# Optimization experiments

Measured on AMD Instinct MI355X. Metric: run time of the kernel, lower is better.

## Reference

```python
import jax, jax.numpy as jnp
import numpy as np
import math

NUM_HEADS = 32
NUM_KV = 8
D = 128          # num_hidden == per-head dim in this module
S = 2048
B = 1
DK = 128
ROPE_BASE = 10000.0


def rope(x):
    # x: [B, H, S, D]; standard Llama-style RoPE (split-halves rotation) over positions.
    d = x.shape[-1]
    half = d // 2
    pos = jnp.arange(x.shape[2], dtype=jnp.float32)                       # [S]
    inv_freq = 1.0 / (ROPE_BASE ** (jnp.arange(half, dtype=jnp.float32) / half))
    ang = pos[:, None] * inv_freq[None, :]                                # [S, half]
    cos = jnp.cos(ang)
    sin = jnp.sin(ang)
    x1 = x[..., :half]
    x2 = x[..., half:]
    return jnp.concatenate([x1 * cos - x2 * sin, x1 * sin + x2 * cos], axis=-1)


def setup_inputs() -> dict:
    key = jax.random.key(0)
    ks = jax.random.split(key, 8)
    query = jax.random.normal(ks[0], (B, S, D), dtype=jnp.float32)
    k_in = jax.random.normal(ks[1], (B, S, D), dtype=jnp.float32)
    v_in = jax.random.normal(ks[2], (B, S, D), dtype=jnp.float32)
    # causal mask: 1 where attention allowed (lower triangle incl diagonal)
    mask = jnp.tril(jnp.ones((S, S), dtype=jnp.int32))[None, None]        # [1,1,S,S]
    sc = 0.02
    Wq = jax.random.normal(ks[3], (NUM_HEADS * D, D), dtype=jnp.float32) * sc
    bq = jnp.zeros((NUM_HEADS * D,), dtype=jnp.float32)
    Wk = jax.random.normal(ks[4], (NUM_KV * D, D), dtype=jnp.float32) * sc
    bk = jnp.zeros((NUM_KV * D,), dtype=jnp.float32)
    Wv = jax.random.normal(ks[5], (NUM_KV * D, D), dtype=jnp.float32) * sc
    bv = jnp.zeros((NUM_KV * D,), dtype=jnp.float32)
    Wo = jax.random.normal(ks[6], (D, NUM_HEADS * D), dtype=jnp.float32) * sc
    bo = jnp.zeros((D,), dtype=jnp.float32)
    return {"query": query, "key": k_in, "values": v_in, "mask": mask,
            "Wq": Wq, "bq": bq, "Wk": Wk, "bk": bk, "Wv": Wv, "bv": bv,
            "Wo": Wo, "bo": bo}


def reference(query, key, values, mask, Wq, bq, Wk, bk, Wv, bv, Wo, bo):
    Bq, Sq, Dh = query.shape
    # projections; torch Linear: x @ W.T + b. Note: view (reshape), not transpose,
    # exactly as in the original module.
    q = (query @ Wq.T + bq).reshape(Bq, NUM_HEADS, Sq, Dh)   # [B,H,S,D]
    k = (key @ Wk.T + bk).reshape(Bq, NUM_KV, Sq, Dh)        # [B,Hkv,S,D]
    v = (values @ Wv.T + bv).reshape(Bq, NUM_KV, Sq, Dh)
    rk = rope(k)
    rv = rope(v)  # module applies RoPE to values too (faithful)
    rep = NUM_HEADS // NUM_KV
    # torch .repeat((1, rep, 1, 1)) tiles whole head blocks -> jnp.tile
    rk = jnp.tile(rk, (1, rep, 1, 1))                        # [B,H,S,D]
    rv = jnp.tile(rv, (1, rep, 1, 1))
    scores = jnp.einsum('bhqd,bhkd->bhqk', q, rk) / math.sqrt(DK)
    scores = jnp.where(mask == 0, -jnp.inf, scores)
    attn = jax.nn.softmax(scores, axis=-1)
    out = jnp.einsum('bhqk,bhkd->bhqd', attn, rv)            # [B,H,S,D]
    out = out.transpose(0, 2, 1, 3).reshape(Bq, Sq, NUM_HEADS * Dh)
    return out @ Wo.T + bo
```

## Files before the change

### kernel.cpp

```cpp
#include <hip/hip_runtime.h>

typedef unsigned short u16;
typedef unsigned int u32;
typedef short frag_t __attribute__((ext_vector_type(8)));
typedef float f32x4 __attribute__((ext_vector_type(4)));

#define S_LEN 2048

__device__ __forceinline__ float bf2f(u32 u) {
  union { u32 i; float f; } v; v.i = u << 16; return v.f;
}
__device__ __forceinline__ u16 f2bf(float f) {
  u32 x = __float_as_uint(f);
  u32 r = (x + 0x7fffu + ((x >> 16) & 1u)) >> 16;
  return (u16)r;
}
__device__ __forceinline__ void unpack8(uint4 r, float* o) {
  o[0] = bf2f(r.x & 0xffffu); o[1] = bf2f(r.x >> 16);
  o[2] = bf2f(r.y & 0xffffu); o[3] = bf2f(r.y >> 16);
  o[4] = bf2f(r.z & 0xffffu); o[5] = bf2f(r.z >> 16);
  o[6] = bf2f(r.w & 0xffffu); o[7] = bf2f(r.w >> 16);
}
__device__ __forceinline__ u16 ld_in(const void* p, size_t idx, bool fp32) {
  if (fp32) return f2bf(((const float*)p)[idx]);
  return ((const u16*)p)[idx];
}
__device__ __forceinline__ uint4 ld8(const void* p, size_t eidx, bool fp32) {
  if (!fp32) return *(const uint4*)((const u16*)p + eidx);
  const float4* f = (const float4*)((const float*)p + eidx);
  float4 x = f[0], y = f[1];
  uint4 r;
  r.x = (u32)f2bf(x.x) | ((u32)f2bf(x.y) << 16);
  r.y = (u32)f2bf(x.z) | ((u32)f2bf(x.w) << 16);
  r.z = (u32)f2bf(y.x) | ((u32)f2bf(y.y) << 16);
  r.w = (u32)f2bf(y.z) | ((u32)f2bf(y.w) << 16);
  return r;
}

__global__ __launch_bounds__(256) void proj_all(
    const void* __restrict__ query, const void* __restrict__ key,
    const void* __restrict__ values,
    const void* __restrict__ Wq, const void* __restrict__ bq,
    const void* __restrict__ Wk, const void* __restrict__ bk,
    const void* __restrict__ Wv, const void* __restrict__ bv,
    u16* __restrict__ Qb, u16* __restrict__ Kb, u16* __restrict__ Vtmp,
    u32* __restrict__ flag_out) {
  __shared__ u16 As[128][136];
  __shared__ u16 Ws[128][136];
  __shared__ u32 flagS;
  u16 (*Cs)[136] = As;
  const int t = threadIdx.x;
  if (t < 64) {
    u32 e = ((u32)((const u16*)query)[2 * t] >> 7) & 0xFFu;
    bool ok = (e >= 110u && e <= 140u);
    unsigned long long b = __ballot(ok);
    if (t == 0) flagS = (__popcll(b) < 32) ? 1u : 0u;
  }
  __syncthreads();
  const bool fp32 = (flagS != 0u);
  if (t == 0 && blockIdx.x == 0 && blockIdx.y == 0) *flag_out = flagS;
  const int x = blockIdx.x;
  const void *A, *W, *bias;
  u16* C; int N, n0;
  if (x < 32)      { A = query;  W = Wq; bias = bq; C = Qb;   N = 4096; n0 = x << 7; }
  else if (x < 40) { A = key;    W = Wk; bias = bk; C = Kb;   N = 1024; n0 = (x - 32) << 7; }
  else             { A = values; W = Wv; bias = bv; C = Vtmp; N = 1024; n0 = (x - 40) << 7; }
  const float osc = (x < 32) ? 0.12751743f : 1.0f;
  const int m0 = blockIdx.y << 7;
#pragma unroll
  for (int i = 0; i < 8; ++i) {
    int task = t + (i << 8);
    int row = task >> 4, ch = (task & 15) << 3;
    *(uint4*)&As[row][ch] = ld8(A, (size_t)(m0 + row) * 128 + ch, fp32);
    *(uint4*)&Ws[row][ch] = ld8(W, (size_t)(n0 + row) * 128 + ch, fp32);
  }
  __syncthreads();
  const int lane = t & 63, w = t >> 6, quad = lane >> 4, l15 = lane & 15;
  const int rm = (w & 1) << 6, rn = (w >> 1) << 6;
  f32x4 acc[4][4];
#pragma unroll
  for (int mt = 0; mt < 4; ++mt)
#pragma unroll
    for (int nt = 0; nt < 4; ++nt) acc[mt][nt] = 0.f;
#pragma unroll
  for (int mtp = 0; mtp < 2; ++mtp) {
    frag_t a0[4], a1[4];
#pragma unroll
    for (int kc = 0; kc < 4; ++kc) {
      a0[kc] = *(const frag_t*)&As[rm + mtp * 32 + l15][kc * 32 + quad * 8];
      a1[kc] = *(const frag_t*)&As[rm + mtp * 32 + 16 + l15][kc * 32 + quad * 8];
    }
#pragma unroll
    for (int nt = 0; nt < 4; ++nt)
#pragma unroll
      for (int kc = 0; kc < 4; ++kc) {
        frag_t b = *(const frag_t*)&Ws[rn + nt * 16 + l15][kc * 32 + quad * 8];
        acc[mtp * 2][nt] = __builtin_amdgcn_mfma_f32_16x16x32_bf16(a0[kc], b, acc[mtp * 2][nt], 0, 0, 0);
        acc[mtp * 2 + 1][nt] = __builtin_amdgcn_mfma_f32_16x16x32_bf16(a1[kc], b, acc[mtp * 2 + 1][nt], 0, 0, 0);
      }
  }
  __syncthreads();
#pragma unroll
  for (int nt = 0; nt < 4; ++nt) {
    float bb = bf2f((u32)ld_in(bias, n0 + rn + nt * 16 + l15, fp32));
#pragma unroll
    for (int mt = 0; mt < 4; ++mt) {
      int row = rm + ((mt >> 1) * 32) + ((mt & 1) * 16) + quad * 4;
#pragma unroll
      for (int r = 0; r < 4; ++r)
        Cs[row + r][rn + nt * 16 + l15] = f2bf((acc[mt][nt][r] + bb) * osc);
    }
  }
  __syncthreads();
#pragma unroll
  for (int i = 0; i < 8; ++i) {
    int task = t + (i << 8);
    int row = task >> 4, ch = (task & 15) << 3;
    *(uint4*)&C[(size_t)(m0 + row) * N + n0 + ch] = *(const uint4*)&Cs[row][ch];
  }
}

__global__ __launch_bounds__(256) void rope_kv_tr(u16* __restrict__ Kb,
                                                  const u16* __restrict__ Vb,
                                                  u16* __restrict__ VbT) {
  __shared__ u16 Lt[128][72];
  const int t = threadIdx.x;
  const int s0 = blockIdx.x << 6;
  const int g = blockIdx.y;
  for (int i = t; i < 4096; i += 256) {
    int s = s0 + (i >> 6), ii = i & 63;
    float invf = __expf(-(float)ii * 0.14391156831212787f);
    float ang = (float)s * invf;
    float sn, cs;
    sincosf(ang, &sn, &cs);
    size_t base = ((size_t)(g << 11) + s) * 128 + ii;
    float k1 = bf2f((u32)Kb[base]), k2 = bf2f((u32)Kb[base + 64]);
    Kb[base] = f2bf(k1 * cs - k2 * sn);
    Kb[base + 64] = f2bf(k1 * sn + k2 * cs);
  }
  const u16* src = Vb + (size_t)g * S_LEN * 128;
  for (int i = t; i < 512; i += 256) {
    int r = i >> 3, d8 = (i & 7) << 3;
    float lo[8], hi[8];
    unpack8(*(const uint4*)&src[(size_t)(s0 + r) * 128 + d8], lo);
    unpack8(*(const uint4*)&src[(size_t)(s0 + r) * 128 + d8 + 64], hi);
#pragma unroll
    for (int j = 0; j < 8; ++j) {
      float invf = __expf(-(float)(d8 + j) * 0.14391156831212787f);
      float ang = (float)(s0 + r) * invf;
      float sn, cs;
      sincosf(ang, &sn, &cs);
      Lt[d8 + j][r] = f2bf(lo[j] * cs - hi[j] * sn);
      Lt[d8 + 64 + j][r] = f2bf(lo[j] * sn + hi[j] * cs);
    }
  }
  __syncthreads();
  u16* dst = VbT + (size_t)g * 128 * S_LEN + s0;
  for (int i = t; i < 2048; i += 256) {
    int d = i >> 4, s4 = (i & 15) << 2;
    uint2 pk;
    pk.x = (u32)Lt[d][s4] | ((u32)Lt[d][s4 + 1] << 16);
    pk.y = (u32)Lt[d][s4 + 2] | ((u32)Lt[d][s4 + 3] << 16);
    *(uint2*)&dst[(size_t)d * S_LEN + s4] = pk;
  }
}

__global__ __launch_bounds__(256) void attn_mfma(
    const u16* __restrict__ Qb, const u16* __restrict__ Kb,
    const u16* __restrict__ VbT, u16* __restrict__ OpA, u16* __restrict__ OpB,
    float2* __restrict__ Ml, int nkh) {
  __shared__ union SmemU {
    struct { u16 Kt[32][136]; u16 Vt[128][40]; u16 St[128][40]; } m;
    struct { u16 Og[128][136]; } e;
  } su;
  const int t = threadIdx.x;
  const int lane = t & 63, w = t >> 6, quad = lane >> 4, l15 = lane & 15;
  const int g = (int)blockIdx.x & 7;
  const int kh = (int)blockIdx.x >> 3;
  const int h = g + (w << 3);
  const u16* Kg = Kb + (size_t)g * S_LEN * 128;
  const u16* Vg = VbT + (size_t)g * 128 * S_LEN;
  const int kR = t >> 4, kC = (t & 15) << 3;
  const int vR = t >> 2, vC = (t & 3) << 3;
  u16* dst = kh ? OpB : OpA;

  const int qt = 63 - (int)blockIdx.y;
  const int q0 = qt << 5;
  const int niter = qt + 1;
  frag_t aq[2][4];
#pragma unroll
  for (int qp = 0; qp < 2; ++qp)
#pragma unroll
    for (int kc = 0; kc < 4; ++kc)
      aq[qp][kc] = *(const frag_t*)&Qb[((size_t)h * S_LEN + q0 + qp * 16 + l15) * 128 +
                                       kc * 32 + quad * 8];
  float m_r[2] = {-1e30f, -1e30f}, l_r[2] = {0.f, 0.f};
  f32x4 oacc[2][8];
#pragma unroll
  for (int qp = 0; qp < 2; ++qp)
#pragma unroll
    for (int nt = 0; nt < 8; ++nt) oacc[qp][nt] = 0.f;

  uint4 kpf[2], vpf[2];
  if (kh < niter) {
    const int k0 = kh << 5;
    kpf[0] = *(const uint4*)&Kg[(size_t)(k0 + kR) * 128 + kC];
    kpf[1] = *(const uint4*)&Kg[(size_t)(k0 + kR + 16) * 128 + kC];
    vpf[0] = *(const uint4*)&Vg[(size_t)vR * S_LEN + k0 + vC];
    vpf[1] = *(const uint4*)&Vg[(size_t)(vR + 64) * S_LEN + k0 + vC];
  }
  for (int sj = kh; sj < niter; sj += nkh) {
    const int k0 = sj << 5;
    __syncthreads();
    *(uint4*)&su.m.Kt[kR][kC] = kpf[0];
    *(uint4*)&su.m.Kt[kR + 16][kC] = kpf[1];
    *(uint4*)&su.m.Vt[vR][vC] = vpf[0];
    *(uint4*)&su.m.Vt[vR + 64][vC] = vpf[1];
    __syncthreads();
    if (sj + nkh < niter) {
      const int kn = (sj + nkh) << 5;
      kpf[0] = *(const uint4*)&Kg[(size_t)(kn + kR) * 128 + kC];
      kpf[1] = *(const uint4*)&Kg[(size_t)(kn + kR + 16) * 128 + kC];
      vpf[0] = *(const uint4*)&Vg[(size_t)vR * S_LEN + kn + vC];
      vpf[1] = *(const uint4*)&Vg[(size_t)(vR + 64) * S_LEN + kn + vC];
    }
    f32x4 s4[2][2];
#pragma unroll
    for (int kk = 0; kk < 2; ++kk) { s4[kk][0] = 0.f; s4[kk][1] = 0.f; }
#pragma unroll
    for (int kc = 0; kc < 4; ++kc)
#pragma unroll
      for (int kk = 0; kk < 2; ++kk) {
        frag_t a = *(const frag_t*)&su.m.Kt[kk * 16 + l15][kc * 32 + quad * 8];
        s4[kk][0] = __builtin_amdgcn_mfma_f32_16x16x32_bf16(a, aq[0][kc], s4[kk][0], 0, 0, 0);
        s4[kk][1] = __builtin_amdgcn_mfma_f32_16x16x32_bf16(a, aq[1][kc], s4[kk][1], 0, 0, 0);
      }
    const bool lastm = (sj == niter - 1);
    float alpha[2];
#pragma unroll
    for (int qp = 0; qp < 2; ++qp) {
      const int qg = q0 + qp * 16 + l15;
      float mx = -1e30f;
#pragma unroll
      for (int kk = 0; kk < 2; ++kk)
#pragma unroll
        for (int r = 0; r < 4; ++r) {
          float sv = s4[kk][qp][r];
          if (lastm && (k0 + kk * 16 + quad * 4 + r) > qg) sv = -1e30f;
          s4[kk][qp][r] = sv;
          mx = fmaxf(mx, sv);
        }
      mx = fmaxf(mx, __shfl_xor(mx, 16));
      mx = fmaxf(mx, __shfl_xor(mx, 32));
      float mn = fmaxf(m_r[qp], mx);
      alpha[qp] = __builtin_amdgcn_exp2f(m_r[qp] - mn);
      m_r[qp] = mn;
      float sum = 0.f;
      const int strow = w * 32 + qp * 16 + l15;
#pragma unroll
      for (int kk = 0; kk < 2; ++kk) {
        float p0 = __builtin_amdgcn_exp2f(s4[kk][qp][0] - mn);
        float p1 = __builtin_amdgcn_exp2f(s4[kk][qp][1] - mn);
        float p2 = __builtin_amdgcn_exp2f(s4[kk][qp][2] - mn);
        float p3 = __builtin_amdgcn_exp2f(s4[kk][qp][3] - mn);
        sum += (p0 + p1) + (p2 + p3);
        uint2 pk;
        pk.x = (u32)f2bf(p0) | ((u32)f2bf(p1) << 16);
        pk.y = (u32)f2bf(p2) | ((u32)f2bf(p3) << 16);
        *(uint2*)&su.m.St[strow][kk * 16 + quad * 4] = pk;
      }
      sum += __shfl_xor(sum, 16);
      sum += __shfl_xor(sum, 32);
      l_r[qp] = l_r[qp] * alpha[qp] + sum;
    }
    if (__any(alpha[0] < 1.0f || alpha[1] < 1.0f)) {
#pragma unroll
      for (int qp = 0; qp < 2; ++qp)
#pragma unroll
        for (int r = 0; r < 4; ++r) {
          float al = __shfl(alpha[qp], quad * 4 + r);
#pragma unroll
          for (int nt = 0; nt < 8; ++nt) oacc[qp][nt][r] *= al;
        }
    }
    frag_t pa0 = *(const frag_t*)&su.m.St[w * 32 + l15][quad * 8];
    frag_t pa1 = *(const frag_t*)&su.m.St[w * 32 + 16 + l15][quad * 8];
#pragma unroll
    for (int nt = 0; nt < 8; ++nt) {
      frag_t v = *(const frag_t*)&su.m.Vt[nt * 16 + l15][quad * 8];
      oacc[0][nt] = __builtin_amdgcn_mfma_f32_16x16x32_bf16(pa0, v, oacc[0][nt], 0, 0, 0);
      oacc[1][nt] = __builtin_amdgcn_mfma_f32_16x16x32_bf16(pa1, v, oacc[1][nt], 0, 0, 0);
    }
  }
  __syncthreads();
#pragma unroll
  for (int qp = 0; qp < 2; ++qp)
#pragma unroll
    for (int r = 0; r < 4; ++r) {
      float fac = 1.0f;
      if (nkh == 1) fac = 1.0f / __shfl(l_r[qp], quad * 4 + r);
      int row = w * 32 + qp * 16 + quad * 4 + r;
#pragma unroll
      for (int nt = 0; nt < 8; ++nt)
        su.e.Og[row][nt * 16 + l15] = f2bf(oacc[qp][nt][r] * fac);
    }
  __syncthreads();
#pragma unroll
  for (int jj = 0; jj < 8; ++jj) {
    int c = t + (jj << 8);
    int row = c >> 4, ch = (c & 15) << 3;
    int hh = row >> 5, qr = row & 31;
    *(uint4*)&dst[(size_t)(q0 + qr) * 4096 + (g + hh * 8) * 128 + ch] =
        *(const uint4*)&su.e.Og[row][ch];
  }
  if (nkh == 2 && quad == 0) {
#pragma unroll
    for (int qp = 0; qp < 2; ++qp)
      Ml[((size_t)kh * 32 + h) * S_LEN + q0 + qp * 16 + l15] =
          make_float2(m_r[qp], l_r[qp]);
  }
}

__global__ __launch_bounds__(256) void out_part(
    const u16* __restrict__ OpA, const u16* __restrict__ OpB,
    const float2* __restrict__ Ml, const void* __restrict__ Wo,
    float* __restrict__ Pout, const u32* __restrict__ flagp, int nkh) {
  __shared__ u16 As[128][136];
  __shared__ u16 Ws[128][136];
  const bool fp32 = (*flagp != 0u);
  const int t = threadIdx.x;
  const int lane = t & 63, w = t >> 6, quad = lane >> 4, l15 = lane & 15;
  const int rm = (w & 1) << 6, rn = (w >> 1) << 6;
  const int m0 = (int)blockIdx.x << 7;
  const int z = (int)blockIdx.y;
  f32x4 acc[4][4];
#pragma unroll
  for (int mt = 0; mt < 4; ++mt)
#pragma unroll
    for (int nt = 0; nt < 4; ++nt) acc[mt][nt] = 0.f;
  for (int kc2 = 0; kc2 < 2; ++kc2) {
    if (kc2) __syncthreads();
    const int kc0 = (z << 8) + (kc2 << 7);
    const int hh = kc0 >> 7;
#pragma unroll
    for (int i = 0; i < 8; ++i) {
      int task = t + (i << 8);
      int row = task >> 4, ch = (task & 15) << 3;
      size_t idx = (size_t)(m0 + row) * 4096 + kc0 + ch;
      if (nkh == 2) {
        int s = m0 + row;
        float2 p1 = Ml[(size_t)hh * S_LEN + s];
        float2 p2 = Ml[(size_t)(32 + hh) * S_LEN + s];
        float mn = fmaxf(p1.x, p2.x);
        float a1 = __builtin_amdgcn_exp2f(p1.x - mn);
        float a2 = __builtin_amdgcn_exp2f(p2.x - mn);
        float linv = 1.0f / (a1 * p1.y + a2 * p2.y);
        float w1 = a1 * linv, w2 = a2 * linv;
        float o1[8], o2[8];
        unpack8(*(const uint4*)&OpA[idx], o1);
        unpack8(*(const uint4*)&OpB[idx], o2);
        uint4 r;
        r.x = (u32)f2bf(o1[0] * w1 + o2[0] * w2) | ((u32)f2bf(o1[1] * w1 + o2[1] * w2) << 16);
        r.y = (u32)f2bf(o1[2] * w1 + o2[2] * w2) | ((u32)f2bf(o1[3] * w1 + o2[3] * w2) << 16);
        r.z = (u32)f2bf(o1[4] * w1 + o2[4] * w2) | ((u32)f2bf(o1[5] * w1 + o2[5] * w2) << 16);
        r.w = (u32)f2bf(o1[6] * w1 + o2[6] * w2) | ((u32)f2bf(o1[7] * w1 + o2[7] * w2) << 16);
        *(uint4*)&As[row][ch] = r;
      } else {
        *(uint4*)&As[row][ch] = *(const uint4*)&OpA[idx];
      }
      *(uint4*)&Ws[row][ch] = ld8(Wo, (size_t)row * 4096 + kc0 + ch, fp32);
    }
    __syncthreads();
#pragma unroll
    for (int mtp = 0; mtp < 2; ++mtp) {
      frag_t a0[4], a1[4];
#pragma unroll
      for (int kc = 0; kc < 4; ++kc) {
        a0[kc] = *(const frag_t*)&As[rm + mtp * 32 + l15][kc * 32 + quad * 8];
        a1[kc] = *(const frag_t*)&As[rm + mtp * 32 + 16 + l15][kc * 32 + quad * 8];
      }
#pragma unroll
      for (int nt = 0; nt < 4; ++nt)
#pragma unroll
        for (int kc = 0; kc < 4; ++kc) {
          frag_t b = *(const frag_t*)&Ws[rn + nt * 16 + l15][kc * 32 + quad * 8];
          acc[mtp * 2][nt] = __builtin_amdgcn_mfma_f32_16x16x32_bf16(a0[kc], b, acc[mtp * 2][nt], 0, 0, 0);
          acc[mtp * 2 + 1][nt] = __builtin_amdgcn_mfma_f32_16x16x32_bf16(a1[kc], b, acc[mtp * 2 + 1][nt], 0, 0, 0);
        }
    }
  }
#pragma unroll
  for (int mt = 0; mt < 4; ++mt) {
    int mrow = m0 + rm + ((mt >> 1) * 32) + ((mt & 1) * 16) + quad * 4;
#pragma unroll
    for (int nt = 0; nt < 4; ++nt) {
      int n = rn + nt * 16 + l15;
#pragma unroll
      for (int r = 0; r < 4; ++r)
        Pout[((size_t)z * 2048 + mrow + r) * 128 + n] = acc[mt][nt][r];
    }
  }
}

__global__ __launch_bounds__(256) void out_red(
    const float* __restrict__ Pout, const void* __restrict__ bo,
    void* __restrict__ out, const u32* __restrict__ flagp) {
  const bool fp32 = (*flagp != 0u);
  int e4 = blockIdx.x * 256 + threadIdx.x;
  const float4* P = (const float4*)Pout;
  float4 s = P[e4];
#pragma unroll
  for (int z = 1; z < 16; ++z) {
    float4 p = P[(size_t)z * 65536 + e4];
    s.x += p.x; s.y += p.y; s.z += p.z; s.w += p.w;
  }
  int n = (e4 << 2) & 127;
  s.x += bf2f((u32)ld_in(bo, n + 0, fp32));
  s.y += bf2f((u32)ld_in(bo, n + 1, fp32));
  s.z += bf2f((u32)ld_in(bo, n + 2, fp32));
  s.w += bf2f((u32)ld_in(bo, n + 3, fp32));
  if (fp32) {
    ((float4*)out)[e4] = s;
  } else {
    uint2 pk;
    pk.x = (u32)f2bf(s.x) | ((u32)f2bf(s.y) << 16);
    pk.y = (u32)f2bf(s.z) | ((u32)f2bf(s.w) << 16);
    *(uint2*)((u16*)out + (e4 << 2)) = pk;
  }
}

extern "C" void kernel_launch(void* const* d_in, const int* in_sizes, int n_in,
                              void* d_out, int out_size, void* d_ws, size_t ws_size,
                              hipStream_t stream) {
  (void)in_sizes; (void)n_in; (void)out_size;
  const void* query  = d_in[0];
  const void* key    = d_in[1];
  const void* values = d_in[2];
  const void* Wq = d_in[4];
  const void* bq = d_in[5];
  const void* Wk = d_in[6];
  const void* bk = d_in[7];
  const void* Wv = d_in[8];
  const void* bv = d_in[9];
  const void* Wo = d_in[10];
  const void* bo = d_in[11];

  char* ws = (char*)d_ws;
  u32* flag   = (u32*)ws;
  u16* Qb     = (u16*)(ws + 64);
  u16* Kb     = (u16*)(ws + 64 + (16ull << 20));
  u16* VbT    = (u16*)(ws + 64 + (20ull << 20));
  u16* Vtmp   = (u16*)(ws + 64 + (24ull << 20));
  u16* Ob     = (u16*)(ws + 64 + (24ull << 20));
  u16* OpB    = (u16*)(ws + 64 + (40ull << 20));
  float2* Mlb = (float2*)(ws + 64 + (56ull << 20));
  float* Pout = (float*)Qb;

  const bool split = (ws_size >= (58ull << 20));
  const int nkh = split ? 2 : 1;

  proj_all<<<dim3(48, 16), 256, 0, stream>>>(query, key, values, Wq, bq, Wk, bk,
                                             Wv, bv, Qb, Kb, Vtmp, flag);
  rope_kv_tr<<<dim3(32, 8), 256, 0, stream>>>(Kb, Vtmp, VbT);
  attn_mfma<<<dim3(8 * nkh, 64), 256, 0, stream>>>(Qb, Kb, VbT, Ob, OpB, Mlb, nkh);
  out_part<<<dim3(16, 16), 256, 0, stream>>>(Ob, OpB, Mlb, Wo, Pout, flag, nkh);
  out_red<<<256, 256, 0, stream>>>(Pout, bo, d_out, flag);
}
```

Before: 248.3 us.

## Pair causal query tiles per attention block, halve out_part tile, use packed bf16 convert

Each attention block now processes two query tiles (qt and 63-qt) in sequence so every block does a balanced amount of causal work, and the grid is halved. Launch bounds request two blocks per SM. The output projection kernel uses 64-row M tiles with twice as many blocks to improve occupancy. Software bf16 rounding is replaced with the hardware v_cvt_pk_bf16_f32 packed conversion. The trade-off is fewer attention blocks, which lowers parallelism and adds a serial second pass inside each block.

```diff
diff --git a/kernel.cpp b/kernel.cpp
--- a/kernel.cpp
+++ b/kernel.cpp
@@ -14,6 +14,11 @@
   u32 x = __float_as_uint(f);
   u32 r = (x + 0x7fffu + ((x >> 16) & 1u)) >> 16;
   return (u16)r;
+}
+__device__ __forceinline__ u32 pkbf(float lo, float hi) {
+  u32 r;
+  asm("v_cvt_pk_bf16_f32 %0, %1, %2" : "=v"(r) : "v"(lo), "v"(hi));
+  return r;
 }
 __device__ __forceinline__ void unpack8(uint4 r, float* o) {
   o[0] = bf2f(r.x & 0xffffu); o[1] = bf2f(r.x >> 16);
@@ -30,10 +35,10 @@
   const float4* f = (const float4*)((const float*)p + eidx);
   float4 x = f[0], y = f[1];
   uint4 r;
-  r.x = (u32)f2bf(x.x) | ((u32)f2bf(x.y) << 16);
-  r.y = (u32)f2bf(x.z) | ((u32)f2bf(x.w) << 16);
-  r.z = (u32)f2bf(y.x) | ((u32)f2bf(y.y) << 16);
-  r.w = (u32)f2bf(y.z) | ((u32)f2bf(y.w) << 16);
+  r.x = pkbf(x.x, x.y);
+  r.y = pkbf(x.z, x.w);
+  r.z = pkbf(y.x, y.y);
+  r.w = pkbf(y.z, y.w);
   return r;
 }
 
@@ -165,7 +170,7 @@
   }
 }
 
-__global__ __launch_bounds__(256) void attn_mfma(
+__global__ __launch_bounds__(256, 2) void attn_mfma(
     const u16* __restrict__ Qb, const u16* __restrict__ Kb,
     const u16* __restrict__ VbT, u16* __restrict__ OpA, u16* __restrict__ OpB,
     float2* __restrict__ Ml, int nkh) {
@@ -177,6 +182,7 @@
   const int lane = t & 63, w = t >> 6, quad = lane >> 4, l15 = lane & 15;
   const int g = (int)blockIdx.x & 7;
   const int kh = (int)blockIdx.x >> 3;
+  const int pi = (int)blockIdx.y;
   const int h = g + (w << 3);
   const u16* Kg = Kb + (size_t)g * S_LEN * 128;
   const u16* Vg = VbT + (size_t)g * 128 * S_LEN;
@@ -184,140 +190,142 @@
   const int vR = t >> 2, vC = (t & 3) << 3;
   u16* dst = kh ? OpB : OpA;
 
-  const int qt = 63 - (int)blockIdx.y;
-  const int q0 = qt << 5;
-  const int niter = qt + 1;
-  frag_t aq[2][4];
-#pragma unroll
-  for (int qp = 0; qp < 2; ++qp)
-#pragma unroll
-    for (int kc = 0; kc < 4; ++kc)
-      aq[qp][kc] = *(const frag_t*)&Qb[((size_t)h * S_LEN + q0 + qp * 16 + l15) * 128 +
-                                       kc * 32 + quad * 8];
-  float m_r[2] = {-1e30f, -1e30f}, l_r[2] = {0.f, 0.f};
-  f32x4 oacc[2][8];
-#pragma unroll
-  for (int qp = 0; qp < 2; ++qp)
-#pragma unroll
-    for (int nt = 0; nt < 8; ++nt) oacc[qp][nt] = 0.f;
-
-  uint4 kpf[2], vpf[2];
-  if (kh < niter) {
-    const int k0 = kh << 5;
-    kpf[0] = *(const uint4*)&Kg[(size_t)(k0 + kR) * 128 + kC];
-    kpf[1] = *(const uint4*)&Kg[(size_t)(k0 + kR + 16) * 128 + kC];
-    vpf[0] = *(const uint4*)&Vg[(size_t)vR * S_LEN + k0 + vC];
-    vpf[1] = *(const uint4*)&Vg[(size_t)(vR + 64) * S_LEN + k0 + vC];
-  }
-  for (int sj = kh; sj < niter; sj += nkh) {
-    const int k0 = sj << 5;
+  for (int tp = 0; tp < 2; ++tp) {
+    const int qt = tp ? pi : 63 - pi;
+    const int q0 = qt << 5;
+    const int niter = qt + 1;
+    frag_t aq[2][4];
+#pragma unroll
+    for (int qp = 0; qp < 2; ++qp)
+#pragma unroll
+      for (int kc = 0; kc < 4; ++kc)
+        aq[qp][kc] = *(const frag_t*)&Qb[((size_t)h * S_LEN + q0 + qp * 16 + l15) * 128 +
+                                         kc * 32 + quad * 8];
+    float m_r[2] = {-1e30f, -1e30f}, l_r[2] = {0.f, 0.f};
+    f32x4 oacc[2][8];
+#pragma unroll
+    for (int qp = 0; qp < 2; ++qp)
+#pragma unroll
+      for (int nt = 0; nt < 8; ++nt) oacc[qp][nt] = 0.f;
+
+    uint4 kpf[2], vpf[2];
+    if (kh < niter) {
+      const int k0 = kh << 5;
+      kpf[0] = *(const uint4*)&Kg[(size_t)(k0 + kR) * 128 + kC];
+      kpf[1] = *(const uint4*)&Kg[(size_t)(k0 + kR + 16) * 128 + kC];
+      vpf[0] = *(const uint4*)&Vg[(size_t)vR * S_LEN + k0 + vC];
+      vpf[1] = *(const uint4*)&Vg[(size_t)(vR + 64) * S_LEN + k0 + vC];
+    }
+    for (int sj = kh; sj < niter; sj += nkh) {
+      const int k0 = sj << 5;
+      __syncthreads();
+      *(uint4*)&su.m.Kt[kR][kC] = kpf[0];
+      *(uint4*)&su.m.Kt[kR + 16][kC] = kpf[1];
+      *(uint4*)&su.m.Vt[vR][vC] = vpf[0];
+      *(uint4*)&su.m.Vt[vR + 64][vC] = vpf[1];
+      __syncthreads();
+      if (sj + nkh < niter) {
+        const int kn = (sj + nkh) << 5;
+        kpf[0] = *(const uint4*)&Kg[(size_t)(kn + kR) * 128 + kC];
+        kpf[1] = *(const uint4*)&Kg[(size_t)(kn + kR + 16) * 128 + kC];
+        vpf[0] = *(const uint4*)&Vg[(size_t)vR * S_LEN + kn + vC];
+        vpf[1] = *(const uint4*)&Vg[(size_t)(vR + 64) * S_LEN + kn + vC];
+      }
+      f32x4 s4[2][2];
+#pragma unroll
+      for (int kk = 0; kk < 2; ++kk) { s4[kk][0] = 0.f; s4[kk][1] = 0.f; }
+#pragma unroll
+      for (int kc = 0; kc < 4; ++kc)
+#pragma unroll
+        for (int kk = 0; kk < 2; ++kk) {
+          frag_t a = *(const frag_t*)&su.m.Kt[kk * 16 + l15][kc * 32 + quad * 8];
+          s4[kk][0] = __builtin_amdgcn_mfma_f32_16x16x32_bf16(a, aq[0][kc], s4[kk][0], 0, 0, 0);
+          s4[kk][1] = __builtin_amdgcn_mfma_f32_16x16x32_bf16(a, aq[1][kc], s4[kk][1], 0, 0, 0);
+        }
+      const bool lastm = (sj == niter - 1);
+      float alpha[2];
+#pragma unroll
+      for (int qp = 0; qp < 2; ++qp) {
+        const int qg = q0 + qp * 16 + l15;
+        float mx = -1e30f;
+#pragma unroll
+        for (int kk = 0; kk < 2; ++kk)
+#pragma unroll
+          for (int r = 0; r < 4; ++r) {
+            float sv = s4[kk][qp][r];
+            if (lastm && (k0 + kk * 16 + quad * 4 + r) > qg) sv = -1e30f;
+            s4[kk][qp][r] = sv;
+            mx = fmaxf(mx, sv);
+          }
+        mx = fmaxf(mx, __shfl_xor(mx, 16));
+        mx = fmaxf(mx, __shfl_xor(mx, 32));
+        float mn = fmaxf(m_r[qp], mx);
+        alpha[qp] = __builtin_amdgcn_exp2f(m_r[qp] - mn);
+        m_r[qp] = mn;
+        float sum = 0.f;
+        const int strow = w * 32 + qp * 16 + l15;
+#pragma unroll
+        for (int kk = 0; kk < 2; ++kk) {
+          float p0 = __builtin_amdgcn_exp2f(s4[kk][qp][0] - mn);
+          float p1 = __builtin_amdgcn_exp2f(s4[kk][qp][1] - mn);
+          float p2 = __builtin_amdgcn_exp2f(s4[kk][qp][2] - mn);
+          float p3 = __builtin_amdgcn_exp2f(s4[kk][qp][3] - mn);
+          sum += (p0 + p1) + (p2 + p3);
+          uint2 pk;
+          pk.x = pkbf(p0, p1);
+          pk.y = pkbf(p2, p3);
+          *(uint2*)&su.m.St[strow][kk * 16 + quad * 4] = pk;
+        }
+        sum += __shfl_xor(sum, 16);
+        sum += __shfl_xor(sum, 32);
+        l_r[qp] = l_r[qp] * alpha[qp] + sum;
+      }
+      if (__any(alpha[0] < 1.0f || alpha[1] < 1.0f)) {
+#pragma unroll
+        for (int qp = 0; qp < 2; ++qp)
+#pragma unroll
+          for (int r = 0; r < 4; ++r) {
+            float al = __shfl(alpha[qp], quad * 4 + r);
+#pragma unroll
+            for (int nt = 0; nt < 8; ++nt) oacc[qp][nt][r] *= al;
+          }
+      }
+      frag_t pa0 = *(const frag_t*)&su.m.St[w * 32 + l15][quad * 8];
+      frag_t pa1 = *(const frag_t*)&su.m.St[w * 32 + 16 + l15][quad * 8];
+#pragma unroll
+      for (int nt = 0; nt < 8; ++nt) {
+        frag_t v = *(const frag_t*)&su.m.Vt[nt * 16 + l15][quad * 8];
+        oacc[0][nt] = __builtin_amdgcn_mfma_f32_16x16x32_bf16(pa0, v, oacc[0][nt], 0, 0, 0);
+        oacc[1][nt] = __builtin_amdgcn_mfma_f32_16x16x32_bf16(pa1, v, oacc[1][nt], 0, 0, 0);
+      }
+    }
     __syncthreads();
-    *(uint4*)&su.m.Kt[kR][kC] = kpf[0];
-    *(uint4*)&su.m.Kt[kR + 16][kC] = kpf[1];
-    *(uint4*)&su.m.Vt[vR][vC] = vpf[0];
-    *(uint4*)&su.m.Vt[vR + 64][vC] = vpf[1];
+#pragma unroll
+    for (int qp = 0; qp < 2; ++qp)
+#pragma unroll
+      for (int r = 0; r < 4; ++r) {
+        float fac = 1.0f;
+        if (nkh == 1) fac = 1.0f / __shfl(l_r[qp], quad * 4 + r);
+        int row = w * 32 + qp * 16 + quad * 4 + r;
+#pragma unroll
+        for (int nt = 0; nt < 8; ++nt)
+          su.e.Og[row][nt * 16 + l15] = f2bf(oacc[qp][nt][r] * fac);
+      }
     __syncthreads();
-    if (sj + nkh < niter) {
-      const int kn = (sj + nkh) << 5;
-      kpf[0] = *(const uint4*)&Kg[(size_t)(kn + kR) * 128 + kC];
-      kpf[1] = *(const uint4*)&Kg[(size_t)(kn + kR + 16) * 128 + kC];
-      vpf[0] = *(const uint4*)&Vg[(size_t)vR * S_LEN + kn + vC];
-      vpf[1] = *(const uint4*)&Vg[(size_t)(vR + 64) * S_LEN + kn + vC];
-    }
-    f32x4 s4[2][2];
-#pragma unroll
-    for (int kk = 0; kk < 2; ++kk) { s4[kk][0] = 0.f; s4[kk][1] = 0.f; }
-#pragma unroll
-    for (int kc = 0; kc < 4; ++kc)
-#pragma unroll
-      for (int kk = 0; kk < 2; ++kk) {
-        frag_t a = *(const frag_t*)&su.m.Kt[kk * 16 + l15][kc * 32 + quad * 8];
-        s4[kk][0] = __builtin_amdgcn_mfma_f32_16x16x32_bf16(a, aq[0][kc], s4[kk][0], 0, 0, 0);
-        s4[kk][1] = __builtin_amdgcn_mfma_f32_16x16x32_bf16(a, aq[1][kc], s4[kk][1], 0, 0, 0);
-      }
-    const bool lastm = (sj == niter - 1);
-    float alpha[2];
-#pragma unroll
-    for (int qp = 0; qp < 2; ++qp) {
-      const int qg = q0 + qp * 16 + l15;
-      float mx = -1e30f;
-#pragma unroll
-      for (int kk = 0; kk < 2; ++kk)
-#pragma unroll
-        for (int r = 0; r < 4; ++r) {
-          float sv = s4[kk][qp][r];
-          if (lastm && (k0 + kk * 16 + quad * 4 + r) > qg) sv = -1e30f;
-          s4[kk][qp][r] = sv;
-          mx = fmaxf(mx, sv);
-        }
-      mx = fmaxf(mx, __shfl_xor(mx, 16));
-      mx = fmaxf(mx, __shfl_xor(mx, 32));
-      float mn = fmaxf(m_r[qp], mx);
-      alpha[qp] = __builtin_amdgcn_exp2f(m_r[qp] - mn);
-      m_r[qp] = mn;
-      float sum = 0.f;
-      const int strow = w * 32 + qp * 16 + l15;
-#pragma unroll
-      for (int kk = 0; kk < 2; ++kk) {
-        float p0 = __builtin_amdgcn_exp2f(s4[kk][qp][0] - mn);
-        float p1 = __builtin_amdgcn_exp2f(s4[kk][qp][1] - mn);
-        float p2 = __builtin_amdgcn_exp2f(s4[kk][qp][2] - mn);
-        float p3 = __builtin_amdgcn_exp2f(s4[kk][qp][3] - mn);
-        sum += (p0 + p1) + (p2 + p3);
-        uint2 pk;
-        pk.x = (u32)f2bf(p0) | ((u32)f2bf(p1) << 16);
-        pk.y = (u32)f2bf(p2) | ((u32)f2bf(p3) << 16);
-        *(uint2*)&su.m.St[strow][kk * 16 + quad * 4] = pk;
-      }
-      sum += __shfl_xor(sum, 16);
-      sum += __shfl_xor(sum, 32);
-      l_r[qp] = l_r[qp] * alpha[qp] + sum;
-    }
-    if (__any(alpha[0] < 1.0f || alpha[1] < 1.0f)) {
+#pragma unroll
+    for (int jj = 0; jj < 8; ++jj) {
+      int c = t + (jj << 8);
+      int row = c >> 4, ch = (c & 15) << 3;
+      int hh = row >> 5, qr = row & 31;
+      *(uint4*)&dst[(size_t)(q0 + qr) * 4096 + (g + hh * 8) * 128 + ch] =
+          *(const uint4*)&su.e.Og[row][ch];
+    }
+    if (nkh == 2 && quad == 0) {
 #pragma unroll
       for (int qp = 0; qp < 2; ++qp)
-#pragma unroll
-        for (int r = 0; r < 4; ++r) {
-          float al = __shfl(alpha[qp], quad * 4 + r);
-#pragma unroll
-          for (int nt = 0; nt < 8; ++nt) oacc[qp][nt][r] *= al;
-        }
-    }
-    frag_t pa0 = *(const frag_t*)&su.m.St[w * 32 + l15][quad * 8];
-    frag_t pa1 = *(const frag_t*)&su.m.St[w * 32 + 16 + l15][quad * 8];
-#pragma unroll
-    for (int nt = 0; nt < 8; ++nt) {
-      frag_t v = *(const frag_t*)&su.m.Vt[nt * 16 + l15][quad * 8];
-      oacc[0][nt] = __builtin_amdgcn_mfma_f32_16x16x32_bf16(pa0, v, oacc[0][nt], 0, 0, 0);
-      oacc[1][nt] = __builtin_amdgcn_mfma_f32_16x16x32_bf16(pa1, v, oacc[1][nt], 0, 0, 0);
-    }
-  }
-  __syncthreads();
-#pragma unroll
-  for (int qp = 0; qp < 2; ++qp)
-#pragma unroll
-    for (int r = 0; r < 4; ++r) {
-      float fac = 1.0f;
-      if (nkh == 1) fac = 1.0f / __shfl(l_r[qp], quad * 4 + r);
-      int row = w * 32 + qp * 16 + quad * 4 + r;
-#pragma unroll
-      for (int nt = 0; nt < 8; ++nt)
-        su.e.Og[row][nt * 16 + l15] = f2bf(oacc[qp][nt][r] * fac);
-    }
-  __syncthreads();
-#pragma unroll
-  for (int jj = 0; jj < 8; ++jj) {
-    int c = t + (jj << 8);
-    int row = c >> 4, ch = (c & 15) << 3;
-    int hh = row >> 5, qr = row & 31;
-    *(uint4*)&dst[(size_t)(q0 + qr) * 4096 + (g + hh * 8) * 128 + ch] =
-        *(const uint4*)&su.e.Og[row][ch];
-  }
-  if (nkh == 2 && quad == 0) {
-#pragma unroll
-    for (int qp = 0; qp < 2; ++qp)
-      Ml[((size_t)kh * 32 + h) * S_LEN + q0 + qp * 16 + l15] =
-          make_float2(m_r[qp], l_r[qp]);
+        Ml[((size_t)kh * 32 + h) * S_LEN + q0 + qp * 16 + l15] =
+            make_float2(m_r[qp], l_r[qp]);
+    }
   }
 }
 
@@ -325,17 +333,17 @@
     const u16* __restrict__ OpA, const u16* __restrict__ OpB,
     const float2* __restrict__ Ml, const void* __restrict__ Wo,
     float* __restrict__ Pout, const u32* __restrict__ flagp, int nkh) {
-  __shared__ u16 As[128][136];
+  __shared__ u16 As[64][136];
   __shared__ u16 Ws[128][136];
   const bool fp32 = (*flagp != 0u);
   const int t = threadIdx.x;
   const int lane = t & 63, w = t >> 6, quad = lane >> 4, l15 = lane & 15;
-  const int rm = (w & 1) << 6, rn = (w >> 1) << 6;
-  const int m0 = (int)blockIdx.x << 7;
+  const int rm = (w & 1) << 5, rn = (w >> 1) << 6;
+  const int m0 = (int)blockIdx.x << 6;
   const int z = (int)blockIdx.y;
-  f32x4 acc[4][4];
-#pragma unroll
-  for (int mt = 0; mt < 4; ++mt)
+  f32x4 acc[2][4];
+#pragma unroll
+  for (int mt = 0; mt < 2; ++mt)
 #pragma unroll
     for (int nt = 0; nt < 4; ++nt) acc[mt][nt] = 0.f;
   for (int kc2 = 0; kc2 < 2; ++kc2) {
@@ -344,6 +352,12 @@
     const int hh = kc0 >> 7;
 #pragma unroll
     for (int i = 0; i < 8; ++i) {
+      int task = t + (i << 8);
+      int row = task >> 4, ch = (task & 15) << 3;
+      *(uint4*)&Ws[row][ch] = ld8(Wo, (size_t)row * 4096 + kc0 + ch, fp32);
+    }
+#pragma unroll
+    for (int i = 0; i < 4; ++i) {
       int task = t + (i << 8);
       int row = task >> 4, ch = (task & 15) << 3;
       size_t idx = (size_t)(m0 + row) * 4096 + kc0 + ch;
@@ -360,38 +374,34 @@
         unpack8(*(const uint4*)&OpA[idx], o1);
         unpack8(*(const uint4*)&OpB[idx], o2);
         uint4 r;
-        r.x = (u32)f2bf(o1[0] * w1 + o2[0] * w2) | ((u32)f2bf(o1[1] * w1 + o2[1] * w2) << 16);
-        r.y = (u32)f2bf(o1[2] * w1 + o2[2] * w2) | ((u32)f2bf(o1[3] * w1 + o2[3] * w2) << 16);
-        r.z = (u32)f2bf(o1[4] * w1 + o2[4] * w2) | ((u32)f2bf(o1[5] * w1 + o2[5] * w2) << 16);
-        r.w = (u32)f2bf(o1[6] * w1 + o2[6] * w2) | ((u32)f2bf(o1[7] * w1 + o2[7] * w2) << 16);
+        r.x = pkbf(o1[0] * w1 + o2[0] * w2, o1[1] * w1 + o2[1] * w2);
+        r.y = pkbf(o1[2] * w1 + o2[2] * w2, o1[3] * w1 + o2[3] * w2);
+        r.z = pkbf(o1[4] * w1 + o2[4] * w2, o1[5] * w1 + o2[5] * w2);
+        r.w = pkbf(o1[6] * w1 + o2[6] * w2, o1[7] * w1 + o2[7] * w2);
         *(uint4*)&As[row][ch] = r;
       } else {
         *(uint4*)&As[row][ch] = *(const uint4*)&OpA[idx];
       }
-      *(uint4*)&Ws[row][ch] = ld8(Wo, (size_t)row * 4096 + kc0 + ch, fp32);
     }
     __syncthreads();
-#pragma unroll
-    for (int mtp = 0; mtp < 2; ++mtp) {
-      frag_t a0[4], a1[4];
+    frag_t a0[4], a1[4];
+#pragma unroll
+    for (int kc = 0; kc < 4; ++kc) {
+      a0[kc] = *(const frag_t*)&As[rm + l15][kc * 32 + quad * 8];
+      a1[kc] = *(const frag_t*)&As[rm + 16 + l15][kc * 32 + quad * 8];
+    }
+#pragma unroll
+    for (int nt = 0; nt < 4; ++nt)
 #pragma unroll
       for (int kc = 0; kc < 4; ++kc) {
-        a0[kc] = *(const frag_t*)&As[rm + mtp * 32 + l15][kc * 32 + quad * 8];
-        a1[kc] = *(const frag_t*)&As[rm + mtp * 32 + 16 + l15][kc * 32 + quad * 8];
-      }
-#pragma unroll
-      for (int nt = 0; nt < 4; ++nt)
-#pragma unroll
-        for (int kc = 0; kc < 4; ++kc) {
-          frag_t b = *(const frag_t*)&Ws[rn + nt * 16 + l15][kc * 32 + quad * 8];
-          acc[mtp * 2][nt] = __builtin_amdgcn_mfma_f32_16x16x32_bf16(a0[kc], b, acc[mtp * 2][nt], 0, 0, 0);
-          acc[mtp * 2 + 1][nt] = __builtin_amdgcn_mfma_f32_16x16x32_bf16(a1[kc], b, acc[mtp * 2 + 1][nt], 0, 0, 0);
-        }
-    }
-  }
-#pragma unroll
-  for (int mt = 0; mt < 4; ++mt) {
-    int mrow = m0 + rm + ((mt >> 1) * 32) + ((mt & 1) * 16) + quad * 4;
+        frag_t b = *(const frag_t*)&Ws[rn + nt * 16 + l15][kc * 32 + quad * 8];
+        acc[0][nt] = __builtin_amdgcn_mfma_f32_16x16x32_bf16(a0[kc], b, acc[0][nt], 0, 0, 0);
+        acc[1][nt] = __builtin_amdgcn_mfma_f32_16x16x32_bf16(a1[kc], b, acc[1][nt], 0, 0, 0);
+      }
+  }
+#pragma unroll
+  for (int mt = 0; mt < 2; ++mt) {
+    int mrow = m0 + rm + mt * 16 + quad * 4;
 #pragma unroll
     for (int nt = 0; nt < 4; ++nt) {
       int n = rn + nt * 16 + l15;
@@ -423,8 +433,8 @@
     ((float4*)out)[e4] = s;
   } else {
     uint2 pk;
-    pk.x = (u32)f2bf(s.x) | ((u32)f2bf(s.y) << 16);
-    pk.y = (u32)f2bf(s.z) | ((u32)f2bf(s.w) << 16);
+    pk.x = pkbf(s.x, s.y);
+    pk.y = pkbf(s.z, s.w);
     *(uint2*)((u16*)out + (e4 << 2)) = pk;
   }
 }
@@ -462,7 +472,7 @@
   proj_all<<<dim3(48, 16), 256, 0, stream>>>(query, key, values, Wq, bq, Wk, bk,
                                              Wv, bv, Qb, Kb, Vtmp, flag);
   rope_kv_tr<<<dim3(32, 8), 256, 0, stream>>>(Kb, Vtmp, VbT);
-  attn_mfma<<<dim3(8 * nkh, 64), 256, 0, stream>>>(Qb, Kb, VbT, Ob, OpB, Mlb, nkh);
-  out_part<<<dim3(16, 16), 256, 0, stream>>>(Ob, OpB, Mlb, Wo, Pout, flag, nkh);
+  attn_mfma<<<dim3(8 * nkh, 32), 256, 0, stream>>>(Qb, Kb, VbT, Ob, OpB, Mlb, nkh);
+  out_part<<<dim3(32, 16), 256, 0, stream>>>(Ob, OpB, Mlb, Wo, Pout, flag, nkh);
   out_red<<<256, 256, 0, stream>>>(Pout, bo, d_out, flag);
 }
```

New measurement: 239.3 us. 1.04x faster.
